# Optimization experiments

Measured on AMD Instinct MI355X. Metric: run time of the kernel, lower is better.

The kernel has to match this reference:

```python
import jax, jax.numpy as jnp
import numpy as np

N_HEAD, D_MODEL, D_HEAD = 16, 1024, 64
SEQ, BATCH = 2048, 2
EPS = 1e-5


def layer_norm(x, g, b):
    mu = jnp.mean(x, axis=-1, keepdims=True)
    var = jnp.var(x, axis=-1, keepdims=True)
    return (x - mu) * jax.lax.rsqrt(var + EPS) * g + b


def pos_table(n_rows, d_model):
    pos = jnp.arange(n_rows, dtype=jnp.float32)[:, None]
    freqs = jnp.power(10000.0, -jnp.arange(0, d_model, 2, dtype=jnp.float32) / d_model)
    ang = pos * freqs  # [n_rows, d_model//2]
    tab = jnp.zeros((n_rows, d_model), dtype=jnp.float32)
    tab = tab.at[:, 0::2].set(jnp.sin(ang))
    tab = tab.at[:, 1::2].set(jnp.cos(ang))
    return tab


def setup_inputs() -> dict:
    key = jax.random.key(0)
    ks = jax.random.split(key, 7)
    s = 0.02
    return {
        "dec_inp": jax.random.normal(ks[0], (SEQ, BATCH, D_MODEL), jnp.float32),
        "Wq": jax.random.normal(ks[1], (N_HEAD * D_HEAD, D_MODEL), jnp.float32) * s,
        "Wkv": jax.random.normal(ks[2], (2 * N_HEAD * D_HEAD, D_MODEL), jnp.float32) * s,
        "Wo": jax.random.normal(ks[3], (D_MODEL, N_HEAD * D_HEAD), jnp.float32) * s,
        "g1": jnp.ones((D_MODEL,), jnp.float32),
        "b1": jnp.zeros((D_MODEL,), jnp.float32),
        "Wff": jax.random.normal(ks[4], (D_MODEL, N_HEAD * D_HEAD), jnp.float32) * s,
        "g2": jnp.ones((D_MODEL,), jnp.float32),
        "b2": jnp.zeros((D_MODEL,), jnp.float32),
    }


def reference(dec_inp, Wq, Wkv, Wo, g1, b1, Wff, g2, b2):
    S, B, D = dec_inp.shape
    scale = 1.0 / (D_HEAD ** 0.5)
    # projections (post-lnorm path, no mems: c == h)
    q = jnp.einsum('ibd,ed->ibe', dec_inp, Wq).reshape(S, B, N_HEAD, D_HEAD)
    kv = jnp.einsum('ibd,ed->ibe', dec_inp, Wkv)
    k, v = jnp.split(kv, 2, axis=-1)
    k = k.reshape(S, B, N_HEAD, D_HEAD)
    v = v.reshape(S, B, N_HEAD, D_HEAD)
    # attention: scores [i, j, b, n], softmax over j (dim=1)
    scores = jnp.einsum('ibnd,jbnd->ijbn', q, k) * scale
    prob = jax.nn.softmax(scores, axis=1)
    vec = jnp.einsum('ijbn,jbnd->ibnd', prob, v).reshape(S, B, N_HEAD * D_HEAD)
    attn_out = jnp.einsum('ibe,de->ibd', vec, Wo)
    out = layer_norm(dec_inp + attn_out, g1, b1)
    # output += ff(output)
    out = out + jnp.einsum('ibe,de->ibd', out, Wff)
    out = layer_norm(out, g2, b2)
    # output += pos_emb(output)  ==  2*out + pe  (pe indexed by shape[1]==batch)
    pe = pos_table(B, D)  # [B, D], broadcasts over seq
    return out + (out + pe)
```

## Files before the change

kernel.cpp:

```cpp
#include <hip/hip_runtime.h>
#include <hip/hip_bf16.h>
#include <math.h>


typedef __bf16 bf16x8 __attribute__((ext_vector_type(8)));
typedef float f32x4  __attribute__((ext_vector_type(4)));

typedef const __attribute__((address_space(1))) unsigned int as1_uint;
typedef __attribute__((address_space(3))) unsigned int as3_uint;

constexpr int S_SEQ = 2048;
constexpr int DH    = 64;

#define WS_MB (1ull << 20)

__device__ __forceinline__ void gload16(void* lds, const void* g) {
  __builtin_amdgcn_global_load_lds((as1_uint*)g, (as3_uint*)lds, 16, 0, 0);
}

__device__ __forceinline__ float fast_exp2(float x) {
  float r;
  asm volatile("v_exp_f32 %0, %1\n\ts_nop 1" : "=v"(r) : "v"(x));
  return r;
}
__device__ __forceinline__ unsigned cvt_pk_bf16(float lo, float hi) {
  unsigned r;
  asm("v_cvt_pk_bf16_f32 %0, %1, %2" : "=v"(r) : "v"(lo), "v"(hi));
  return r;
}

__device__ __forceinline__ void cvt4(const float* __restrict__ in,
                                     __hip_bfloat16* __restrict__ out, int idx) {
  float4 v = ((const float4*)in)[idx];
  uint2 p;
  p.x = cvt_pk_bf16(v.x, v.y);
  p.y = cvt_pk_bf16(v.z, v.w);
  *(uint2*)(out + (size_t)idx * 4) = p;
}

__global__ __launch_bounds__(256)
void prep_kernel(const float* __restrict__ x, const float* __restrict__ Wq,
                 const float* __restrict__ Wkv, const float* __restrict__ Wo,
                 const float* __restrict__ Wff,
                 __hip_bfloat16* __restrict__ Xb,
                 __hip_bfloat16* __restrict__ Wqkv_b,
                 __hip_bfloat16* __restrict__ Wo_b,
                 __hip_bfloat16* __restrict__ Wff_b,
                 float* __restrict__ pe) {
  const int bid = blockIdx.x, t = threadIdx.x;
  if (bid < 4096) {
    cvt4(x, Xb, bid * 256 + t);
  } else if (bid < 5120) {
    cvt4(Wq, Wqkv_b, (bid - 4096) * 256 + t);
  } else if (bid < 7168) {
    cvt4(Wkv, Wqkv_b + 1024 * 1024, (bid - 5120) * 256 + t);
  } else if (bid < 8192) {
    cvt4(Wo, Wo_b, (bid - 7168) * 256 + t);
  } else if (bid < 9216) {
    cvt4(Wff, Wff_b, (bid - 8192) * 256 + t);
  } else {
#pragma unroll
    for (int rep = 0; rep < 2; ++rep) {
      const int k = rep * 256 + t;
      float freq = expf(-(2.0f * (float)k / 1024.0f) * logf(10000.0f));
      pe[2 * k]            = 0.0f;
      pe[2 * k + 1]        = 1.0f;
      pe[1024 + 2 * k]     = sinf(freq);
      pe[1024 + 2 * k + 1] = cosf(freq);
    }
  }
}

template <int MODE, int BN>
__global__ __launch_bounds__(256)
void gemm_bt(const __hip_bfloat16* __restrict__ A,
             const __hip_bfloat16* __restrict__ Bw,
             float* __restrict__ C,
             __hip_bfloat16* __restrict__ Qb,
             __hip_bfloat16* __restrict__ Kb,
             __hip_bfloat16* __restrict__ VTb,
             int Ndim, int Kdim) {
  constexpr int ASZ = 128 * 64 * 2;
  constexpr int BSZ = BN * 64 * 2;
  constexpr int NI  = BN / 32;
  __shared__ __align__(16) char smem[2 * (ASZ + BSZ)];
  const int t = threadIdx.x, w = t >> 6, l = t & 63;
  const int bm = blockIdx.y * 128, bn = blockIdx.x * BN;
  const int m0 = (w >> 1) * 64, n0 = (w & 1) * (BN / 2);
  const int lrow = l >> 3, lcol = l & 7;
  const int ll = l & 15, lg = l >> 4;
  const int scol = (lcol ^ lrow) * 8;

  auto stage = [&](char* buf, int kt) {
#pragma unroll
    for (int r = 0; r < 4; ++r) {
      const int chunk = r * 4 + w;
      const int row = chunk * 8 + lrow;
      gload16(buf + chunk * 1024 + l * 16,
              A + (size_t)(bm + row) * Kdim + kt + scol);
    }
#pragma unroll
    for (int r = 0; r < BN / 32; ++r) {
      const int chunk = r * 4 + w;
      const int row = chunk * 8 + lrow;
      gload16(buf + ASZ + chunk * 1024 + l * 16,
              Bw + (size_t)(bn + row) * Kdim + kt + scol);
    }
  };

  f32x4 acc[4][NI] = {};

  stage(smem, 0);
  stage(smem + (ASZ + BSZ), 64);
  const int NST = Kdim / 64;
  for (int kt = 0; kt < NST; ++kt) {
    if (kt < NST - 1) {
      if constexpr (BN == 128)
        asm volatile("s_waitcnt vmcnt(8)" ::: "memory");
      else
        asm volatile("s_waitcnt vmcnt(6)" ::: "memory");
    } else {
      asm volatile("s_waitcnt vmcnt(0)" ::: "memory");
    }
    __builtin_amdgcn_s_barrier();
    char* sA = smem + (kt & 1) * (ASZ + BSZ);
    const char* sB = sA + ASZ;
#pragma unroll
    for (int ks = 0; ks < 2; ++ks) {
      bf16x8 a[4], bfr[NI];
#pragma unroll
      for (int mi = 0; mi < 4; ++mi) {
        const int row = m0 + mi * 16 + ll;
        a[mi] = *(const bf16x8*)(sA + row * 128 +
                                 (((ks * 4 + lg) ^ (ll & 7)) << 4));
      }
#pragma unroll
      for (int ni = 0; ni < NI; ++ni) {
        const int row = n0 + ni * 16 + ll;
        bfr[ni] = *(const bf16x8*)(sB + row * 128 +
                                   (((ks * 4 + lg) ^ (ll & 7)) << 4));
      }
#pragma unroll
      for (int mi = 0; mi < 4; ++mi)
#pragma unroll
        for (int ni = 0; ni < NI; ++ni)
          acc[mi][ni] = __builtin_amdgcn_mfma_f32_16x16x32_bf16(
              a[mi], bfr[ni], acc[mi][ni], 0, 0, 0);
    }
    if (kt + 2 < NST) {
      __builtin_amdgcn_s_barrier();
      stage(sA, (kt + 2) * 64);
    }
  }

  if (MODE == 0) {
#pragma unroll
    for (int mi = 0; mi < 4; ++mi)
#pragma unroll
      for (int ni = 0; ni < NI; ++ni)
#pragma unroll
        for (int r = 0; r < 4; ++r) {
          const int gm = bm + m0 + mi * 16 + lg * 4 + r;
          const int gn = bn + n0 + ni * 16 + ll;
          C[(size_t)gm * Ndim + gn] = acc[mi][ni][r];
        }
  } else {
    __syncthreads();
    __hip_bfloat16* img = (__hip_bfloat16*)smem;
    const bool isV = (bn >= 2048);
#pragma unroll
    for (int mi = 0; mi < 4; ++mi)
#pragma unroll
      for (int ni = 0; ni < NI; ++ni)
#pragma unroll
        for (int r = 0; r < 4; ++r) {
          const int gml = m0 + mi * 16 + lg * 4 + r;
          const int gnl = n0 + ni * 16 + ll;
          const int off = isV ? gnl * 136 + ((gml & 1) << 6) + (gml >> 1)
                              : gml * 136 + gnl;
          img[off] = __float2bfloat16(acc[mi][ni][r]);
        }
    __syncthreads();
    const int i0 = bm >> 1;
    const int tile0 = bm >> 6;
#pragma unroll
    for (int j = 0; j < 8; ++j) {
      const int c = j * 256 + t;
      uint4 val;
      __hip_bfloat16* dst;
      if (bn < 1024) {
        const int bb = c >> 10, hl = (c >> 9) & 1;
        const int q = c & 511, il = q >> 3, dh0 = (q & 7) * 8;
        val = *(const uint4*)&img[(il * 2 + bb) * 136 + hl * 64 + dh0];
        dst = Qb + ((size_t)(bb * 16 + (bn >> 6) + hl) * 2048 + i0 + il) * 64 + dh0;
      } else if (bn < 2048) {
        const int run = c >> 6, lane = c & 63;
        const int bb = run >> 4, hl = (run >> 3) & 1, th = (run >> 2) & 1,
                  instr = run & 3;
        const int lg2 = lane >> 4, ll2 = lane & 15;
        const int r32 = (ll2 >> 2) * 8 + (ll2 & 3) + ((instr >> 1) << 2);
        const int il = th * 32 + r32;
        const int dh0 = (instr & 1) * 32 + lg2 * 8;
        val = *(const uint4*)&img[(il * 2 + bb) * 136 + hl * 64 + dh0];
        dst = Kb + (size_t)(bb * 16 + ((bn - 1024) >> 6) + hl) * 131072 +
              (size_t)(tile0 + th) * 2048 + instr * 512 + lane * 8;
      } else {
        const int run = c >> 6, lane = c & 63;
        const int bb = run >> 4, hl = (run >> 3) & 1, th = (run >> 2) & 1,
                  df = run & 3;
        const int lg2 = lane >> 4, ll2 = lane & 15;
        const int il0 = th * 32 + lg2 * 8;
        const int gnl = hl * 64 + df * 16 + ll2;
        val = *(const uint4*)&img[gnl * 136 + bb * 64 + il0];
        dst = VTb + (size_t)(bb * 16 + ((bn - 2048) >> 6) + hl) * 131072 +
              (size_t)(tile0 + th) * 2048 + df * 512 + lane * 8;
      }
      *(uint4*)dst = val;
    }
  }
}


#define MFMA_B16 __builtin_amdgcn_mfma_f32_16x16x32_bf16

#define STAGE2(bufp, cb)                                                      \
  {                                                                           \
    gload16((bufp) + woff, Kf + (cb) + wl16);                                 \
    gload16((bufp) + 4096 + woff, Vf + (cb) + wl16);                          \
    gload16((bufp) + 8192 + woff, Kf + (cb) + 4096 + wl16);                   \
    gload16((bufp) + 12288 + woff, Vf + (cb) + 4096 + wl16);                  \
  }

#define COMPUTE(cur)                                                          \
  {                                                                           \
    bf16x8 kk[4], vv[4];                                                      \
    _Pragma("unroll")                                                         \
    for (int i = 0; i < 4; ++i) {                                             \
      kk[i] = *(const bf16x8*)((cur) + i * 1024 + l16);                       \
      vv[i] = *(const bf16x8*)((cur) + 4096 + i * 1024 + l16);                \
    }                                                                         \
    const f32x4 z = {0.f, 0.f, 0.f, 0.f};                                     \
    f32x4 s0[2], s1[2];                                                       \
    __builtin_amdgcn_s_setprio(1);                                            \
    s0[0] = MFMA_B16(kk[0], qf[0][0], z, 0, 0, 0);                            \
    s0[0] = MFMA_B16(kk[1], qf[0][1], s0[0], 0, 0, 0);                        \
    s1[0] = MFMA_B16(kk[2], qf[0][0], z, 0, 0, 0);                            \
    s1[0] = MFMA_B16(kk[3], qf[0][1], s1[0], 0, 0, 0);                        \
    s0[1] = MFMA_B16(kk[0], qf[1][0], z, 0, 0, 0);                            \
    s0[1] = MFMA_B16(kk[1], qf[1][1], s0[1], 0, 0, 0);                        \
    s1[1] = MFMA_B16(kk[2], qf[1][0], z, 0, 0, 0);                            \
    s1[1] = MFMA_B16(kk[3], qf[1][1], s1[1], 0, 0, 0);                        \
    __builtin_amdgcn_s_setprio(0);                                            \
    _Pragma("unroll")                                                         \
    for (int qi = 0; qi < 2; ++qi) {                                          \
      float p[8];                                                             \
      _Pragma("unroll")                                                       \
      for (int r = 0; r < 4; ++r) {                                           \
        p[r]     = fast_exp2(s0[qi][r] * C1);                                 \
        p[4 + r] = fast_exp2(s1[qi][r] * C1);                                 \
      }                                                                       \
      union { unsigned u[4]; bf16x8 v; } pk;                                  \
      pk.u[0] = cvt_pk_bf16(p[0], p[1]);                                      \
      pk.u[1] = cvt_pk_bf16(p[2], p[3]);                                      \
      pk.u[2] = cvt_pk_bf16(p[4], p[5]);                                      \
      pk.u[3] = cvt_pk_bf16(p[6], p[7]);                                      \
      __builtin_amdgcn_s_setprio(1);                                          \
      _Pragma("unroll")                                                       \
      for (int df = 0; df < 4; ++df)                                          \
        oacc[qi][df] = MFMA_B16(pk.v, vv[df], oacc[qi][df], 0, 0, 0);         \
      oaccS[qi] = MFMA_B16(pk.v, onesv.v, oaccS[qi], 0, 0, 0);                \
      __builtin_amdgcn_s_setprio(0);                                          \
    }                                                                         \
  }

#define PHASE(curbuf, stgbuf, stgoff, vmN_, doStage_)                         \
  {                                                                           \
    asm volatile("s_waitcnt vmcnt(" #vmN_ ")" ::: "memory");                  \
    __builtin_amdgcn_s_barrier();                                             \
    if (doStage_) STAGE2(stgbuf, stgoff);                                     \
    COMPUTE(curbuf);                                                          \
    COMPUTE((curbuf) + 8192);                                                 \
  }

__global__ __launch_bounds__(256)
void attn_kernel(const __hip_bfloat16* __restrict__ Qb,
                 const __hip_bfloat16* __restrict__ Kb,
                 const __hip_bfloat16* __restrict__ VTb,
                 __hip_bfloat16* __restrict__ vec) {
  __shared__ __align__(16) char lds[3 * 16384];
  const int t = threadIdx.x, w = t >> 6, l = t & 63;
  const int bid = blockIdx.x;
  const int slot = bid >> 3;
  const int bh = (bid & 7) * 4 + (slot & 3);
  const int qt = slot >> 2;
  const int b = bh >> 4, h = bh & 15;
  const __hip_bfloat16* Q = Qb + (size_t)bh * S_SEQ * DH;
  const char* Kf = (const char*)Kb + (size_t)bh * 262144;
  const char* Vf = (const char*)VTb + (size_t)bh * 262144;
  const int ll = l & 15, lg = l >> 4;
  const int l16 = l * 16;
  const int woff = w * 1024 + l16;
  const int wl16 = woff;
  constexpr float C1 = 0.125f * 1.44269504088896f;

  const int qbase = qt * 128 + w * 32;
  bf16x8 qf[2][2];
#pragma unroll
  for (int qi = 0; qi < 2; ++qi) {
    qf[qi][0] = *(const bf16x8*)(Q + (size_t)(qbase + qi * 16 + ll) * 64 + lg * 8);
    qf[qi][1] = *(const bf16x8*)(Q + (size_t)(qbase + qi * 16 + ll) * 64 + 32 + lg * 8);
  }

  union { unsigned u[4]; bf16x8 v; } onesv;
  onesv.u[0] = 0x3F803F80u; onesv.u[1] = 0x3F803F80u;
  onesv.u[2] = 0x3F803F80u; onesv.u[3] = 0x3F803F80u;

  f32x4 oacc[2][4] = {};
  f32x4 oaccS[2] = {};

  char* b0 = lds;
  char* b1 = lds + 16384;
  char* b2 = lds + 32768;

  STAGE2(b0, 0);
  STAGE2(b1, 8192);

  int cb = 2 * 8192;
  for (int i = 0; i < 10; ++i) {
    PHASE(b0, b2, cb, 4, true); cb += 8192;
    PHASE(b1, b0, cb, 4, true); cb += 8192;
    PHASE(b2, b1, cb, 4, true); cb += 8192;
  }
  PHASE(b0, b2, 0, 4, false);
  PHASE(b1, b0, 0, 0, false);

#pragma unroll
  for (int qi = 0; qi < 2; ++qi) {
    float invR[4];
#pragma unroll
    for (int r = 0; r < 4; ++r) invR[r] = 1.0f / oaccS[qi][r];
#pragma unroll
    for (int df = 0; df < 4; ++df)
#pragma unroll
      for (int r = 0; r < 4; ++r) {
        const int row = qbase + qi * 16 + 4 * lg + r;
        const int e = h * 64 + df * 16 + ll;
        vec[((size_t)row * 2 + b) * 1024 + e] =
            __float2bfloat16(oacc[qi][df][r] * invR[r]);
      }
  }
}

__global__ __launch_bounds__(256)
void add_ln_kernel(const float* __restrict__ X, const float* __restrict__ Yadd,
                   const float* __restrict__ g, const float* __restrict__ bb,
                   float* __restrict__ out_f32,
                   __hip_bfloat16* __restrict__ out_b16) {
  const int row = blockIdx.x, t = threadIdx.x;
  const float4 x4 = *(const float4*)(X + (size_t)row * 1024 + t * 4);
  const float4 a4 = *(const float4*)(Yadd + (size_t)row * 1024 + t * 4);
  float v[4] = {x4.x + a4.x, x4.y + a4.y, x4.z + a4.z, x4.w + a4.w};
  float s = v[0] + v[1] + v[2] + v[3];
  float s2 = v[0] * v[0] + v[1] * v[1] + v[2] * v[2] + v[3] * v[3];
#pragma unroll
  for (int off = 1; off < 64; off <<= 1) {
    s += __shfl_xor(s, off);
    s2 += __shfl_xor(s2, off);
  }
  __shared__ float rs[4], rs2[4];
  if ((t & 63) == 0) { rs[t >> 6] = s; rs2[t >> 6] = s2; }
  __syncthreads();
  const float tot = rs[0] + rs[1] + rs[2] + rs[3];
  const float tot2 = rs2[0] + rs2[1] + rs2[2] + rs2[3];
  const float mu = tot * (1.0f / 1024.0f);
  const float var = tot2 * (1.0f / 1024.0f) - mu * mu;
  const float rstd = rsqrtf(var + 1e-5f);
  const float4 g4 = *(const float4*)(g + t * 4);
  const float4 b4 = *(const float4*)(bb + t * 4);
  float y[4];
  y[0] = (v[0] - mu) * rstd * g4.x + b4.x;
  y[1] = (v[1] - mu) * rstd * g4.y + b4.y;
  y[2] = (v[2] - mu) * rstd * g4.z + b4.z;
  y[3] = (v[3] - mu) * rstd * g4.w + b4.w;
  *(float4*)(out_f32 + (size_t)row * 1024 + t * 4) =
      make_float4(y[0], y[1], y[2], y[3]);
  uint2 pk2;
  pk2.x = cvt_pk_bf16(y[0], y[1]);
  pk2.y = cvt_pk_bf16(y[2], y[3]);
  *(uint2*)(out_b16 + (size_t)row * 1024 + t * 4) = pk2;
}

__global__ __launch_bounds__(256)
void final_kernel(const float* __restrict__ X, const float* __restrict__ Yadd,
                  const float* __restrict__ g, const float* __restrict__ bb,
                  const float* __restrict__ pe, float* __restrict__ out) {
  const int row = blockIdx.x, t = threadIdx.x;
  const float4 x4 = *(const float4*)(X + (size_t)row * 1024 + t * 4);
  const float4 a4 = *(const float4*)(Yadd + (size_t)row * 1024 + t * 4);
  float v[4] = {x4.x + a4.x, x4.y + a4.y, x4.z + a4.z, x4.w + a4.w};
  float s = v[0] + v[1] + v[2] + v[3];
  float s2 = v[0] * v[0] + v[1] * v[1] + v[2] * v[2] + v[3] * v[3];
#pragma unroll
  for (int off = 1; off < 64; off <<= 1) {
    s += __shfl_xor(s, off);
    s2 += __shfl_xor(s2, off);
  }
  __shared__ float rs[4], rs2[4];
  if ((t & 63) == 0) { rs[t >> 6] = s; rs2[t >> 6] = s2; }
  __syncthreads();
  const float tot = rs[0] + rs[1] + rs[2] + rs[3];
  const float tot2 = rs2[0] + rs2[1] + rs2[2] + rs2[3];
  const float mu = tot * (1.0f / 1024.0f);
  const float var = tot2 * (1.0f / 1024.0f) - mu * mu;
  const float rstd = rsqrtf(var + 1e-5f);
  const float4 g4 = *(const float4*)(g + t * 4);
  const float4 b4 = *(const float4*)(bb + t * 4);
  const int bidx = row & 1;
  const float4 p4 = *(const float4*)(pe + bidx * 1024 + t * 4);
  float y[4];
  y[0] = 2.0f * ((v[0] - mu) * rstd * g4.x + b4.x) + p4.x;
  y[1] = 2.0f * ((v[1] - mu) * rstd * g4.y + b4.y) + p4.y;
  y[2] = 2.0f * ((v[2] - mu) * rstd * g4.z + b4.z) + p4.z;
  y[3] = 2.0f * ((v[3] - mu) * rstd * g4.w + b4.w) + p4.w;
  *(float4*)(out + (size_t)row * 1024 + t * 4) = make_float4(y[0], y[1], y[2], y[3]);
}

extern "C" void kernel_launch(void* const* d_in, const int* in_sizes, int n_in,
                              void* d_out, int out_size, void* d_ws,
                              size_t ws_size, hipStream_t stream) {
  const float* x   = (const float*)d_in[0];
  const float* Wq  = (const float*)d_in[1];
  const float* Wkv = (const float*)d_in[2];
  const float* Wo  = (const float*)d_in[3];
  const float* g1  = (const float*)d_in[4];
  const float* b1  = (const float*)d_in[5];
  const float* Wff = (const float*)d_in[6];
  const float* g2  = (const float*)d_in[7];
  const float* b2  = (const float*)d_in[8];

  char* ws = (char*)d_ws;
  __hip_bfloat16* Wqkv_b = (__hip_bfloat16*)(ws + 0);
  __hip_bfloat16* Wo_b   = (__hip_bfloat16*)(ws + 6 * WS_MB);
  __hip_bfloat16* Wff_b  = (__hip_bfloat16*)(ws + 8 * WS_MB);
  __hip_bfloat16* Xb     = (__hip_bfloat16*)(ws + 10 * WS_MB);
  __hip_bfloat16* Qb     = (__hip_bfloat16*)(ws + 18 * WS_MB);
  __hip_bfloat16* Kb     = (__hip_bfloat16*)(ws + 26 * WS_MB);
  __hip_bfloat16* VTb    = (__hip_bfloat16*)(ws + 34 * WS_MB);
  __hip_bfloat16* vecb   = (__hip_bfloat16*)(ws + 42 * WS_MB);
  float* attn            = (float*)(ws + 18 * WS_MB);
  float* out1            = (float*)(ws + 50 * WS_MB);
  __hip_bfloat16* out1b  = (__hip_bfloat16*)(ws + 66 * WS_MB);
  float* ffb             = (float*)(ws + 34 * WS_MB);
  float* pe              = (float*)(ws + 74 * WS_MB);

  prep_kernel<<<9217, 256, 0, stream>>>(x, Wq, Wkv, Wo, Wff, Xb, Wqkv_b,
                                        Wo_b, Wff_b, pe);
  gemm_bt<1, 128><<<dim3(24, 32), 256, 0, stream>>>(Xb, Wqkv_b, nullptr, Qb,
                                                    Kb, VTb, 3072, 1024);
  attn_kernel<<<dim3(512), 256, 0, stream>>>(Qb, Kb, VTb, vecb);
  gemm_bt<0, 64><<<dim3(16, 32), 256, 0, stream>>>(vecb, Wo_b, attn, nullptr,
                                                   nullptr, nullptr, 1024, 1024);
  add_ln_kernel<<<4096, 256, 0, stream>>>(x, attn, g1, b1, out1, out1b);
  gemm_bt<0, 64><<<dim3(16, 32), 256, 0, stream>>>(out1b, Wff_b, ffb, nullptr,
                                                   nullptr, nullptr, 1024, 1024);
  final_kernel<<<4096, 256, 0, stream>>>(out1, ffb, g2, b2, pe, (float*)d_out);
}
```

Before: 139.3 us.

## Double per-wave query tile in attention and fold softmax scale into Q

Each attention wave now handles 64 query rows instead of 32, so every K/V tile staged in LDS feeds twice as many MFMAs, and the grid shrinks from 512 to 256 blocks. The score MFMAs are regrouped across four query fragments, and the exp/pack step is split from the PV MFMAs to give the scheduler more independent work. The softmax scale times log2(e) is now applied to Q in the QKV GEMM epilogue before bf16 rounding, which removes a multiply per exponent. The cost is roughly double the accumulator and Q-fragment registers, and only one block per CU, which may reduce latency hiding and adds slight rounding differences in Q.

```diff
diff --git a/kernel.cpp b/kernel.cpp
--- a/kernel.cpp
+++ b/kernel.cpp
@@ -11,6 +11,7 @@
 
 constexpr int S_SEQ = 2048;
 constexpr int DH    = 64;
+constexpr float C1SC = 0.125f * 1.44269504088896f;
 
 #define WS_MB (1ull << 20)
 
@@ -168,6 +169,7 @@
     __syncthreads();
     __hip_bfloat16* img = (__hip_bfloat16*)smem;
     const bool isV = (bn >= 2048);
+    const float qsc = (bn < 1024) ? C1SC : 1.0f;
 #pragma unroll
     for (int mi = 0; mi < 4; ++mi)
 #pragma unroll
@@ -178,7 +180,7 @@
           const int gnl = n0 + ni * 16 + ll;
           const int off = isV ? gnl * 136 + ((gml & 1) << 6) + (gml >> 1)
                               : gml * 136 + gnl;
-          img[off] = __float2bfloat16(acc[mi][ni][r]);
+          img[off] = __float2bfloat16(acc[mi][ni][r] * qsc);
         }
     __syncthreads();
     const int i0 = bm >> 1;
@@ -240,37 +242,42 @@
       vv[i] = *(const bf16x8*)((cur) + 4096 + i * 1024 + l16);                \
     }                                                                         \
     const f32x4 z = {0.f, 0.f, 0.f, 0.f};                                     \
-    f32x4 s0[2], s1[2];                                                       \
+    f32x4 s0[4], s1[4];                                                       \
     __builtin_amdgcn_s_setprio(1);                                            \
-    s0[0] = MFMA_B16(kk[0], qf[0][0], z, 0, 0, 0);                            \
-    s0[0] = MFMA_B16(kk[1], qf[0][1], s0[0], 0, 0, 0);                        \
-    s1[0] = MFMA_B16(kk[2], qf[0][0], z, 0, 0, 0);                            \
-    s1[0] = MFMA_B16(kk[3], qf[0][1], s1[0], 0, 0, 0);                        \
-    s0[1] = MFMA_B16(kk[0], qf[1][0], z, 0, 0, 0);                            \
-    s0[1] = MFMA_B16(kk[1], qf[1][1], s0[1], 0, 0, 0);                        \
-    s1[1] = MFMA_B16(kk[2], qf[1][0], z, 0, 0, 0);                            \
-    s1[1] = MFMA_B16(kk[3], qf[1][1], s1[1], 0, 0, 0);                        \
+    _Pragma("unroll")                                                         \
+    for (int qi = 0; qi < 4; ++qi) {                                          \
+      s0[qi] = MFMA_B16(kk[0], qf[qi][0], z, 0, 0, 0);                        \
+      s1[qi] = MFMA_B16(kk[2], qf[qi][0], z, 0, 0, 0);                        \
+    }                                                                         \
+    _Pragma("unroll")                                                         \
+    for (int qi = 0; qi < 4; ++qi) {                                          \
+      s0[qi] = MFMA_B16(kk[1], qf[qi][1], s0[qi], 0, 0, 0);                   \
+      s1[qi] = MFMA_B16(kk[3], qf[qi][1], s1[qi], 0, 0, 0);                   \
+    }                                                                         \
     __builtin_amdgcn_s_setprio(0);                                            \
+    union { unsigned u[4]; bf16x8 v; } pk[4];                                 \
     _Pragma("unroll")                                                         \
-    for (int qi = 0; qi < 2; ++qi) {                                          \
+    for (int qi = 0; qi < 4; ++qi) {                                          \
       float p[8];                                                             \
       _Pragma("unroll")                                                       \
       for (int r = 0; r < 4; ++r) {                                           \
-        p[r]     = fast_exp2(s0[qi][r] * C1);                                 \
-        p[4 + r] = fast_exp2(s1[qi][r] * C1);                                 \
+        p[r]     = fast_exp2(s0[qi][r]);                                      \
+        p[4 + r] = fast_exp2(s1[qi][r]);                                      \
       }                                                                       \
-      union { unsigned u[4]; bf16x8 v; } pk;                                  \
-      pk.u[0] = cvt_pk_bf16(p[0], p[1]);                                      \
-      pk.u[1] = cvt_pk_bf16(p[2], p[3]);                                      \
-      pk.u[2] = cvt_pk_bf16(p[4], p[5]);                                      \
-      pk.u[3] = cvt_pk_bf16(p[6], p[7]);                                      \
-      __builtin_amdgcn_s_setprio(1);                                          \
+      pk[qi].u[0] = cvt_pk_bf16(p[0], p[1]);                                  \
+      pk[qi].u[1] = cvt_pk_bf16(p[2], p[3]);                                  \
+      pk[qi].u[2] = cvt_pk_bf16(p[4], p[5]);                                  \
+      pk[qi].u[3] = cvt_pk_bf16(p[6], p[7]);                                  \
+    }                                                                         \
+    __builtin_amdgcn_s_setprio(1);                                            \
+    _Pragma("unroll")                                                         \
+    for (int qi = 0; qi < 4; ++qi) {                                          \
       _Pragma("unroll")                                                       \
       for (int df = 0; df < 4; ++df)                                          \
-        oacc[qi][df] = MFMA_B16(pk.v, vv[df], oacc[qi][df], 0, 0, 0);         \
-      oaccS[qi] = MFMA_B16(pk.v, onesv.v, oaccS[qi], 0, 0, 0);                \
-      __builtin_amdgcn_s_setprio(0);                                          \
+        oacc[qi][df] = MFMA_B16(pk[qi].v, vv[df], oacc[qi][df], 0, 0, 0);     \
+      oaccS[qi] = MFMA_B16(pk[qi].v, onesv.v, oaccS[qi], 0, 0, 0);            \
     }                                                                         \
+    __builtin_amdgcn_s_setprio(0);                                            \
   }
 
 #define PHASE(curbuf, stgbuf, stgoff, vmN_, doStage_)                         \
@@ -301,12 +308,11 @@
   const int l16 = l * 16;
   const int woff = w * 1024 + l16;
   const int wl16 = woff;
-  constexpr float C1 = 0.125f * 1.44269504088896f;
-
-  const int qbase = qt * 128 + w * 32;
-  bf16x8 qf[2][2];
-#pragma unroll
-  for (int qi = 0; qi < 2; ++qi) {
+
+  const int qbase = qt * 256 + w * 64;
+  bf16x8 qf[4][2];
+#pragma unroll
+  for (int qi = 0; qi < 4; ++qi) {
     qf[qi][0] = *(const bf16x8*)(Q + (size_t)(qbase + qi * 16 + ll) * 64 + lg * 8);
     qf[qi][1] = *(const bf16x8*)(Q + (size_t)(qbase + qi * 16 + ll) * 64 + 32 + lg * 8);
   }
@@ -315,8 +321,8 @@
   onesv.u[0] = 0x3F803F80u; onesv.u[1] = 0x3F803F80u;
   onesv.u[2] = 0x3F803F80u; onesv.u[3] = 0x3F803F80u;
 
-  f32x4 oacc[2][4] = {};
-  f32x4 oaccS[2] = {};
+  f32x4 oacc[4][4] = {};
+  f32x4 oaccS[4] = {};
 
   char* b0 = lds;
   char* b1 = lds + 16384;
@@ -335,7 +341,7 @@
   PHASE(b1, b0, 0, 0, false);
 
 #pragma unroll
-  for (int qi = 0; qi < 2; ++qi) {
+  for (int qi = 0; qi < 4; ++qi) {
     float invR[4];
 #pragma unroll
     for (int r = 0; r < 4; ++r) invR[r] = 1.0f / oaccS[qi][r];
@@ -457,7 +463,7 @@
                                         Wo_b, Wff_b, pe);
   gemm_bt<1, 128><<<dim3(24, 32), 256, 0, stream>>>(Xb, Wqkv_b, nullptr, Qb,
                                                     Kb, VTb, 3072, 1024);
-  attn_kernel<<<dim3(512), 256, 0, stream>>>(Qb, Kb, VTb, vecb);
+  attn_kernel<<<dim3(256), 256, 0, stream>>>(Qb, Kb, VTb, vecb);
   gemm_bt<0, 64><<<dim3(16, 32), 256, 0, stream>>>(vecb, Wo_b, attn, nullptr,
                                                    nullptr, nullptr, 1024, 1024);
   add_ln_kernel<<<4096, 256, 0, stream>>>(x, attn, g1, b1, out1, out1b);
```

After: 145.0 us. 4.1% more time.
